# Optimization experiments

Hardware: AMD Instinct MI355X
Metric: run time of the kernel (lower is better)

## Reference

```python
import jax, jax.numpy as jnp
import numpy as np

N_EL = 16
N_NUC = 4
N_FEATS = 32
CUTOFF = 10.0
ION_POT = 0.5
ALPHA = 1.0
BATCH = 32768
HIDDEN = 64
I_IDX, J_IDX = np.triu_indices(N_EL, 1)  # electron pairs i<j
N_PAIRS = N_EL * N_NUC + N_EL * (N_EL - 1) // 2
D_IN = N_PAIRS * N_FEATS


def ssp(x):
    # shifted softplus: softplus(x) - log(2), so ssp(0) = 0
    return jax.nn.softplus(x) - jnp.log(2.0).astype(x.dtype)


def setup_inputs() -> dict:
    key = jax.random.key(0)
    ks = jax.random.split(key, 9)
    rs = jax.random.normal(ks[0], (BATCH, N_EL, 3), jnp.float32) * 2.0
    coords = jax.random.normal(ks[1], (N_NUC, 3), jnp.float32)
    charges = jnp.arange(1, N_NUC + 1, dtype=jnp.float32)
    W1 = jax.random.normal(ks[2], (D_IN, HIDDEN), jnp.float32) / jnp.sqrt(D_IN)
    b1 = jnp.zeros((HIDDEN,), jnp.float32)
    W2 = jax.random.normal(ks[3], (HIDDEN, HIDDEN), jnp.float32) / jnp.sqrt(HIDDEN)
    b2 = jnp.zeros((HIDDEN,), jnp.float32)
    W3 = jax.random.normal(ks[4], (HIDDEN, 1), jnp.float32) / jnp.sqrt(HIDDEN)
    b3 = jnp.zeros((1,), jnp.float32)
    return {"rs": rs, "coords": coords, "charges": charges,
            "W1": W1, "b1": b1, "W2": W2, "b2": b2, "W3": W3, "b3": b3}


def reference(rs, coords, charges, W1, b1, W2, b2, W3, b3):
    B = rs.shape[0]
    # electron-nucleus distances: [B, n_el, n_nuc]
    diff_nuc = rs[:, :, None, :] - coords[None, None, :, :]
    dists_nuc = jnp.sqrt(jnp.sum(diff_nuc * diff_nuc, axis=-1))
    # electron-electron distances for pairs i<j: [B, n_el*(n_el-1)//2]
    diff_el = rs[:, I_IDX, :] - rs[:, J_IDX, :]
    dists_el = jnp.sqrt(jnp.sum(diff_el * diff_el, axis=-1))
    dists = jnp.concatenate([dists_nuc.reshape(B, -1), dists_el], axis=1)  # [B, N_PAIRS]
    # Gaussian distance basis expansion
    qs = jnp.linspace(0.0, 1.0, N_FEATS, dtype=rs.dtype)
    mus = CUTOFF * qs ** 2
    sigmas = (1.0 + CUTOFF * qs) / 7.0
    xs = jnp.exp(-((dists[..., None] - mus) ** 2) / sigmas ** 2)  # [B, N_PAIRS, N_FEATS]
    xs = xs.reshape(B, -1)
    # small MLP with shifted-softplus activations
    h = ssp(xs @ W1 + b1)
    h = ssp(h @ W2 + b2)
    ys = (h @ W3 + b3)[:, 0]
    # nuclear asymptotic factor
    decay = jnp.sqrt(2.0 * ION_POT)
    terms = (charges[None, None, :] * dists_nuc + decay * ALPHA * dists_nuc ** 2) / (1.0 + ALPHA * dists_nuc)
    asymp = jnp.exp(-jnp.sum(terms, axis=(1, 2)))
    return jnp.exp(ys) * asymp
```

## Files before the change

kernel.cpp:

```cpp
#include <hip/hip_runtime.h>
#include <math.h>

#define N_EL    16
#define N_NUC   4
#define N_FEATS 32
#define N_PAIRS 184
#define HIDDEN  64
#define TB      32
#define BLOCK   256
#define DLD     185
#define H1LD    68
#define TPW     23
#define WS_PART_OFF (1 << 19)

typedef int   intx8    __attribute__((ext_vector_type(8)));
typedef float floatx16 __attribute__((ext_vector_type(16)));

__constant__ unsigned char c_I[120] = {
    0,0,0,0,0,0,0,0,0,0,0,0,0,0,0,
    1,1,1,1,1,1,1,1,1,1,1,1,1,1,
    2,2,2,2,2,2,2,2,2,2,2,2,2,
    3,3,3,3,3,3,3,3,3,3,3,3,
    4,4,4,4,4,4,4,4,4,4,4,
    5,5,5,5,5,5,5,5,5,5,
    6,6,6,6,6,6,6,6,6,
    7,7,7,7,7,7,7,7,
    8,8,8,8,8,8,8,
    9,9,9,9,9,9,
    10,10,10,10,10,
    11,11,11,11,
    12,12,12,
    13,13,
    14
};
__constant__ unsigned char c_J[120] = {
    1,2,3,4,5,6,7,8,9,10,11,12,13,14,15,
    2,3,4,5,6,7,8,9,10,11,12,13,14,15,
    3,4,5,6,7,8,9,10,11,12,13,14,15,
    4,5,6,7,8,9,10,11,12,13,14,15,
    5,6,7,8,9,10,11,12,13,14,15,
    6,7,8,9,10,11,12,13,14,15,
    7,8,9,10,11,12,13,14,15,
    8,9,10,11,12,13,14,15,
    9,10,11,12,13,14,15,
    10,11,12,13,14,15,
    11,12,13,14,15,
    12,13,14,15,
    13,14,15,
    14,15,
    15
};

__device__ __forceinline__ float ssp(float x) {
    float a = fabsf(x);
    return fmaxf(x, 0.0f) + log1pf(__expf(-a)) - 0.69314718056f;
}
__device__ __forceinline__ float redg(float v) {
    v += __shfl_xor(v, 1);
    v += __shfl_xor(v, 2);
    v += __shfl_xor(v, 4);
    return v;
}

__global__ __launch_bounds__(256)
void prep_w1_kernel(const float* __restrict__ W1, intx8* __restrict__ ws)
{
    __shared__ float w[2 * N_FEATS * HIDDEN];
    const int t = blockIdx.x;
    const float* src = W1 + (size_t)(2 * t) * (N_FEATS * HIDDEN);
    for (int k = threadIdx.x; k < 2 * N_FEATS * HIDDEN; k += 256) w[k] = src[k];
    __syncthreads();

    const int tid = threadIdx.x;
    if (tid >= 128) return;
    const int lane = tid & 63;
    const int nh   = tid >> 6;
    const int lh   = lane >> 5;
    const int col  = nh * 32 + (lane & 31);
    const int fb   = lh * 16;
    intx8 frag;
#pragma unroll
    for (int r = 0; r < 8; ++r) {
        const int pair = r >> 2;
        const int fo   = fb + ((r & 3) << 2);
        const float v0 = 64.0f * w[(pair * N_FEATS + fo + 0) * 64 + col];
        const float v1 = 64.0f * w[(pair * N_FEATS + fo + 1) * 64 + col];
        const float v2 = 64.0f * w[(pair * N_FEATS + fo + 2) * 64 + col];
        const float v3 = 64.0f * w[(pair * N_FEATS + fo + 3) * 64 + col];
        int d = __builtin_amdgcn_cvt_pk_fp8_f32(v0, v1, 0, false);
        d     = __builtin_amdgcn_cvt_pk_fp8_f32(v2, v3, d, true);
        frag[r] = d;
    }
    ws[(size_t)(t * 2 + nh) * 64 + lane] = frag;
}

__global__ __launch_bounds__(BLOCK)
void wfnet_gemm(const float* __restrict__ rs,
                const float* __restrict__ coords,
                const intx8* __restrict__ ws,
                float* __restrict__ partials)
{
    __shared__ float lds_rs[TB * N_EL * 3];
    __shared__ float lds_dist[TB * DLD];

    const int tid  = threadIdx.x;
    const int wave = tid >> 6;
    const int lane = tid & 63;
    const int m    = lane & 31;
    const int lh   = lane >> 5;

    {
        const float* rs_blk = rs + (size_t)blockIdx.x * (TB * N_EL * 3);
        for (int k = tid; k < TB * N_EL * 3; k += BLOCK) lds_rs[k] = rs_blk[k];
    }
    __syncthreads();

    {
        const int bl = tid >> 3, g = tid & 7;
        const float* myrs = lds_rs + bl * (N_EL * 3);
        float* dst = lds_dist + bl * DLD;
        for (int i = 0; i < 8; ++i) {
            const int p = g + 8 * i;
            const int e = p >> 2, n = p & 3;
            const float dx = myrs[e * 3 + 0] - coords[n * 3 + 0];
            const float dy = myrs[e * 3 + 1] - coords[n * 3 + 1];
            const float dz = myrs[e * 3 + 2] - coords[n * 3 + 2];
            dst[p] = sqrtf(dx * dx + dy * dy + dz * dz);
        }
        for (int i = 0; i < 15; ++i) {
            const int q  = g + 8 * i;
            const int ei = 3 * (int)c_I[q], ej = 3 * (int)c_J[q];
            const float dx = myrs[ei + 0] - myrs[ej + 0];
            const float dy = myrs[ei + 1] - myrs[ej + 1];
            const float dz = myrs[ei + 2] - myrs[ej + 2];
            dst[64 + q] = sqrtf(dx * dx + dy * dy + dz * dz);
        }
    }
    __syncthreads();

    const int f0 = lh * 16;
#define MKC(P, FF) float P##1, P##0; { \
    const float fq = (float)(FF) * (1.0f / 31.0f); \
    const float mu = 10.0f * fq * fq; \
    const float is = 7.0f / (1.0f + 10.0f * fq); \
    P##1 = is * 3.3972871404442143f; \
    P##0 = -mu * P##1; }
    MKC(F0_,  f0 + 0)  MKC(F1_,  f0 + 1)  MKC(F2_,  f0 + 2)  MKC(F3_,  f0 + 3)
    MKC(F4_,  f0 + 4)  MKC(F5_,  f0 + 5)  MKC(F6_,  f0 + 6)  MKC(F7_,  f0 + 7)
    MKC(F8_,  f0 + 8)  MKC(F9_,  f0 + 9)  MKC(F10_, f0 + 10) MKC(F11_, f0 + 11)
    MKC(F12_, f0 + 12) MKC(F13_, f0 + 13) MKC(F14_, f0 + 14) MKC(F15_, f0 + 15)
#undef MKC

    floatx16 accA = {};
    floatx16 accB = {};
    const intx8* wq = ws + ((size_t)(wave * TPW) * 128 + lane);
    const float* drow = lds_dist + m * DLD + wave * (2 * TPW);

#define XZ(dd, P) ({ const float t_ = fmaf(dd, P##1, P##0); fmaf(t_, -t_, 56.5f); })
#define PKD(dd, A, B, C, D) ({ \
    unsigned w_; \
    w_ = __builtin_amdgcn_cvt_pk_u8_f32(XZ(dd, A), 0, 0u); \
    w_ = __builtin_amdgcn_cvt_pk_u8_f32(XZ(dd, B), 1, w_); \
    w_ = __builtin_amdgcn_cvt_pk_u8_f32(XZ(dd, C), 2, w_); \
    w_ = __builtin_amdgcn_cvt_pk_u8_f32(XZ(dd, D), 3, w_); \
    (int)w_; })
#define MKA8(AV, dx0, dx1) \
    intx8 AV; { \
    AV[0] = PKD(dx0, F0_,  F1_,  F2_,  F3_);  \
    AV[1] = PKD(dx0, F4_,  F5_,  F6_,  F7_);  \
    AV[2] = PKD(dx0, F8_,  F9_,  F10_, F11_); \
    AV[3] = PKD(dx0, F12_, F13_, F14_, F15_); \
    AV[4] = PKD(dx1, F0_,  F1_,  F2_,  F3_);  \
    AV[5] = PKD(dx1, F4_,  F5_,  F6_,  F7_);  \
    AV[6] = PKD(dx1, F8_,  F9_,  F10_, F11_); \
    AV[7] = PKD(dx1, F12_, F13_, F14_, F15_); }
#define KROUND(AV, Q0, Q1) { \
    accA = __builtin_amdgcn_mfma_scale_f32_32x32x64_f8f6f4( \
               AV, Q0, accA, 0, 0, 0, 0x7F7F7F7F, 0, 0x79797979); \
    accB = __builtin_amdgcn_mfma_scale_f32_32x32x64_f8f6f4( \
               AV, Q1, accB, 0, 0, 0, 0x7F7F7F7F, 0, 0x79797979); }

    intx8 pA0 = wq[0],   pA1 = wq[64];
    intx8 pB0 = wq[128], pB1 = wq[192];
    float dA0 = drow[0], dA1 = drow[1];
    float dB0 = drow[2], dB1 = drow[3];

#pragma unroll 1
    for (int it = 0; it < 10; ++it) {
        const intx8* wn = wq + 256;
        const float eA0 = drow[4 * it + 4], eA1 = drow[4 * it + 5];
        const float eB0 = drow[4 * it + 6], eB1 = drow[4 * it + 7];

        { MKA8(av, dA0, dA1) KROUND(av, pA0, pA1) }
        pA0 = wn[0]; pA1 = wn[64];

        { MKA8(bv, dB0, dB1) KROUND(bv, pB0, pB1) }
        pB0 = wn[128]; pB1 = wn[192];

        wq = wn;
        dA0 = eA0; dA1 = eA1; dB0 = eB0; dB1 = eB1;
    }
    {
        const intx8* wn = wq + 256;
        const float eA0 = drow[44], eA1 = drow[45];
        { MKA8(av, dA0, dA1) KROUND(av, pA0, pA1) }
        pA0 = wn[0]; pA1 = wn[64];
        { MKA8(bv, dB0, dB1) KROUND(bv, pB0, pB1) }
        { MKA8(cv, eA0, eA1) KROUND(cv, pA0, pA1) }
    }
#undef KROUND
#undef MKA8
#undef PKD
#undef XZ

    float* pdst = partials + ((size_t)blockIdx.x * 4 + wave) * 2048;
#pragma unroll
    for (int rg = 0; rg < 16; ++rg) {
        const int el = (rg & 3) + 8 * (rg >> 2) + 4 * lh;
        pdst[el * 64 + m]      = accA[rg];
        pdst[el * 64 + 32 + m] = accB[rg];
    }
}

__global__ __launch_bounds__(BLOCK)
void wfnet_tail(const float* __restrict__ rs,
                const float* __restrict__ coords,
                const float* __restrict__ charges,
                const float* __restrict__ partials,
                const float* __restrict__ b1,
                const float* __restrict__ W2,
                const float* __restrict__ b2,
                const float* __restrict__ W3,
                const float* __restrict__ b3,
                float* __restrict__ out)
{
    __shared__ float lds_rs[TB * N_EL * 3];
    __shared__ float lds_h1[TB * H1LD];
    __shared__ float lds_w2[HIDDEN * HIDDEN];

    const int tid = threadIdx.x;
    const int el  = tid >> 3;
    const int g   = tid & 7;
    const int b   = blockIdx.x * TB + el;

    {
        const float* rs_blk = rs + (size_t)blockIdx.x * (TB * N_EL * 3);
        for (int k = tid; k < TB * N_EL * 3; k += BLOCK) lds_rs[k] = rs_blk[k];
    }
    {
        float4* dst = (float4*)lds_w2;
        const float4* src = (const float4*)W2;
#pragma unroll
        for (int i = 0; i < 4; ++i) dst[tid + 256 * i] = src[tid + 256 * i];
    }

    {
        const float* pb = partials + (size_t)blockIdx.x * 8192 + el * 64 + g * 8;
        const float4 p00 = ((const float4*)(pb + 0 * 2048))[0];
        const float4 p01 = ((const float4*)(pb + 0 * 2048))[1];
        const float4 p10 = ((const float4*)(pb + 1 * 2048))[0];
        const float4 p11 = ((const float4*)(pb + 1 * 2048))[1];
        const float4 p20 = ((const float4*)(pb + 2 * 2048))[0];
        const float4 p21 = ((const float4*)(pb + 2 * 2048))[1];
        const float4 p30 = ((const float4*)(pb + 3 * 2048))[0];
        const float4 p31 = ((const float4*)(pb + 3 * 2048))[1];
        const float4 ba = ((const float4*)(b1 + g * 8))[0];
        const float4 bb = ((const float4*)(b1 + g * 8))[1];
        float* h1w = lds_h1 + el * H1LD + g * 8;
        h1w[0] = ssp(p00.x + p10.x + p20.x + p30.x + ba.x);
        h1w[1] = ssp(p00.y + p10.y + p20.y + p30.y + ba.y);
        h1w[2] = ssp(p00.z + p10.z + p20.z + p30.z + ba.z);
        h1w[3] = ssp(p00.w + p10.w + p20.w + p30.w + ba.w);
        h1w[4] = ssp(p01.x + p11.x + p21.x + p31.x + bb.x);
        h1w[5] = ssp(p01.y + p11.y + p21.y + p31.y + bb.y);
        h1w[6] = ssp(p01.z + p11.z + p21.z + p31.z + bb.z);
        h1w[7] = ssp(p01.w + p11.w + p21.w + p31.w + bb.w);
    }

    float asy = 0.0f;
    __syncthreads();
    {
        const float* myrs = lds_rs + el * (N_EL * 3);
        const float4 ch = *(const float4*)charges;
#pragma unroll
        for (int i = 0; i < 8; ++i) {
            const int p = g + 8 * i;
            const int e = p >> 2, n = p & 3;
            const float dx = myrs[e * 3 + 0] - coords[n * 3 + 0];
            const float dy = myrs[e * 3 + 1] - coords[n * 3 + 1];
            const float dz = myrs[e * 3 + 2] - coords[n * 3 + 2];
            const float d = sqrtf(dx * dx + dy * dy + dz * dz);
            const float Z = (n < 2) ? ((n == 0) ? ch.x : ch.y)
                                    : ((n == 2) ? ch.z : ch.w);
            asy += (Z * d + d * d) / (1.0f + d);
        }
    }
    asy = redg(asy);

    const float4* __restrict__ W2v = (const float4*)lds_w2;
    const float4* __restrict__ b2v = (const float4*)b2;
    const int wbi = g * 2;
    const float4 b2a = b2v[wbi], b2b = b2v[wbi + 1];
    float s0 = b2a.x, s1 = b2a.y, s2 = b2a.z, s3 = b2a.w;
    float s4 = b2b.x, s5 = b2b.y, s6 = b2b.z, s7 = b2b.w;

    const float* __restrict__ h1row = lds_h1 + el * H1LD;
    for (int k = 0; k < HIDDEN; ++k) {
        const float hk  = h1row[k];
        const float4 wa = W2v[k * 16 + wbi];
        const float4 wb = W2v[k * 16 + wbi + 1];
        s0 = fmaf(hk, wa.x, s0); s1 = fmaf(hk, wa.y, s1);
        s2 = fmaf(hk, wa.z, s2); s3 = fmaf(hk, wa.w, s3);
        s4 = fmaf(hk, wb.x, s4); s5 = fmaf(hk, wb.y, s5);
        s6 = fmaf(hk, wb.z, s6); s7 = fmaf(hk, wb.w, s7);
    }

    const float4* __restrict__ W3v = (const float4*)W3;
    const float4 w3a = W3v[wbi], w3b = W3v[wbi + 1];
    float part = ssp(s0) * w3a.x + ssp(s1) * w3a.y
               + ssp(s2) * w3a.z + ssp(s3) * w3a.w
               + ssp(s4) * w3b.x + ssp(s5) * w3b.y
               + ssp(s6) * w3b.z + ssp(s7) * w3b.w;
    part = redg(part);

    if (g == 0) {
        const float ys = part + b3[0];
        out[b] = __expf(ys) * __expf(-asy);
    }
}

extern "C" void kernel_launch(void* const* d_in, const int* in_sizes, int n_in,
                              void* d_out, int out_size, void* d_ws, size_t ws_size,
                              hipStream_t stream) {
    const float* rs      = (const float*)d_in[0];
    const float* coords  = (const float*)d_in[1];
    const float* charges = (const float*)d_in[2];
    const float* W1      = (const float*)d_in[3];
    const float* b1      = (const float*)d_in[4];
    const float* W2      = (const float*)d_in[5];
    const float* b2      = (const float*)d_in[6];
    const float* W3      = (const float*)d_in[7];
    const float* b3      = (const float*)d_in[8];
    float* out = (float*)d_out;

    const int batch = in_sizes[0] / (N_EL * 3);
    intx8* w1f8     = (intx8*)d_ws;
    float* partials = (float*)((char*)d_ws + WS_PART_OFF);

    prep_w1_kernel<<<N_PAIRS / 2, 256, 0, stream>>>(W1, w1f8);
    wfnet_gemm<<<batch / TB, BLOCK, 0, stream>>>(rs, coords, w1f8, partials);
    wfnet_tail<<<batch / TB, BLOCK, 0, stream>>>(rs, coords, charges, partials,
                                                 b1, W2, b2, W3, b3, out);
}
```

Before: 129.9 us.

## Split GEMM K-loop across eight waves per block and reduce eight partials

Doubles the gemm block to 512 threads so each wave handles about half of its former K-tiles, shortening the per-wave serial MFMA chain and adding more waves per block. The explicit software prefetch of weights and distances is dropped in favour of simple in-loop loads. The distance precompute is redistributed over 16 threads per batch row. The tail kernel now sums eight partial slices instead of four, which doubles the partials traffic written and read through global memory.

```diff
diff --git a/kernel.cpp b/kernel.cpp
--- a/kernel.cpp
+++ b/kernel.cpp
@@ -7,7 +7,7 @@
 #define N_PAIRS 184
 #define HIDDEN  64
 #define TB      32
-#define BLOCK   256
+#define BLOCK   512
 #define DLD     185
 #define H1LD    68
 #define TPW     23
@@ -108,6 +108,8 @@
     const int lane = tid & 63;
     const int m    = lane & 31;
     const int lh   = lane >> 5;
+    const int w4   = wave & 3;
+    const int half = wave >> 2;
 
     {
         const float* rs_blk = rs + (size_t)blockIdx.x * (TB * N_EL * 3);
@@ -116,24 +118,28 @@
     __syncthreads();
 
     {
-        const int bl = tid >> 3, g = tid & 7;
+        const int bl = tid >> 4, g = tid & 15;
         const float* myrs = lds_rs + bl * (N_EL * 3);
         float* dst = lds_dist + bl * DLD;
-        for (int i = 0; i < 8; ++i) {
-            const int p = g + 8 * i;
+#pragma unroll
+        for (int i = 0; i < 4; ++i) {
+            const int p = g + 16 * i;
             const int e = p >> 2, n = p & 3;
             const float dx = myrs[e * 3 + 0] - coords[n * 3 + 0];
             const float dy = myrs[e * 3 + 1] - coords[n * 3 + 1];
             const float dz = myrs[e * 3 + 2] - coords[n * 3 + 2];
             dst[p] = sqrtf(dx * dx + dy * dy + dz * dz);
         }
-        for (int i = 0; i < 15; ++i) {
-            const int q  = g + 8 * i;
-            const int ei = 3 * (int)c_I[q], ej = 3 * (int)c_J[q];
-            const float dx = myrs[ei + 0] - myrs[ej + 0];
-            const float dy = myrs[ei + 1] - myrs[ej + 1];
-            const float dz = myrs[ei + 2] - myrs[ej + 2];
-            dst[64 + q] = sqrtf(dx * dx + dy * dy + dz * dz);
+#pragma unroll
+        for (int i = 0; i < 8; ++i) {
+            const int q = g + 16 * i;
+            if (q < 120) {
+                const int ei = 3 * (int)c_I[q], ej = 3 * (int)c_J[q];
+                const float dx = myrs[ei + 0] - myrs[ej + 0];
+                const float dy = myrs[ei + 1] - myrs[ej + 1];
+                const float dz = myrs[ei + 2] - myrs[ej + 2];
+                dst[64 + q] = sqrtf(dx * dx + dy * dy + dz * dz);
+            }
         }
     }
     __syncthreads();
@@ -153,8 +159,9 @@
 
     floatx16 accA = {};
     floatx16 accB = {};
-    const intx8* wq = ws + ((size_t)(wave * TPW) * 128 + lane);
-    const float* drow = lds_dist + m * DLD + wave * (2 * TPW);
+    const intx8* wq = ws + ((size_t)(23 * w4 + 12 * half) * 128 + lane);
+    const float* drow = lds_dist + m * DLD + 46 * w4 + 24 * half;
+    const int nd = 6 - half;
 
 #define XZ(dd, P) ({ const float t_ = fmaf(dd, P##1, P##0); fmaf(t_, -t_, 56.5f); })
 #define PKD(dd, A, B, C, D) ({ \
@@ -180,40 +187,27 @@
     accB = __builtin_amdgcn_mfma_scale_f32_32x32x64_f8f6f4( \
                AV, Q1, accB, 0, 0, 0, 0x7F7F7F7F, 0, 0x79797979); }
 
-    intx8 pA0 = wq[0],   pA1 = wq[64];
-    intx8 pB0 = wq[128], pB1 = wq[192];
-    float dA0 = drow[0], dA1 = drow[1];
-    float dB0 = drow[2], dB1 = drow[3];
-
 #pragma unroll 1
-    for (int it = 0; it < 10; ++it) {
-        const intx8* wn = wq + 256;
-        const float eA0 = drow[4 * it + 4], eA1 = drow[4 * it + 5];
-        const float eB0 = drow[4 * it + 6], eB1 = drow[4 * it + 7];
-
-        { MKA8(av, dA0, dA1) KROUND(av, pA0, pA1) }
-        pA0 = wn[0]; pA1 = wn[64];
-
-        { MKA8(bv, dB0, dB1) KROUND(bv, pB0, pB1) }
-        pB0 = wn[128]; pB1 = wn[192];
-
-        wq = wn;
-        dA0 = eA0; dA1 = eA1; dB0 = eB0; dB1 = eB1;
-    }
-    {
-        const intx8* wn = wq + 256;
-        const float eA0 = drow[44], eA1 = drow[45];
-        { MKA8(av, dA0, dA1) KROUND(av, pA0, pA1) }
-        pA0 = wn[0]; pA1 = wn[64];
-        { MKA8(bv, dB0, dB1) KROUND(bv, pB0, pB1) }
-        { MKA8(cv, eA0, eA1) KROUND(cv, pA0, pA1) }
+    for (int it = 0; it < nd; ++it) {
+        const intx8 a0 = wq[0],   a1 = wq[64];
+        const intx8 b0 = wq[128], b1 = wq[192];
+        const float d0 = drow[4 * it + 0], d1 = drow[4 * it + 1];
+        const float d2 = drow[4 * it + 2], d3 = drow[4 * it + 3];
+        { MKA8(av, d0, d1) KROUND(av, a0, a1) }
+        { MKA8(bv, d2, d3) KROUND(bv, b0, b1) }
+        wq += 256;
+    }
+    if (half) {
+        const intx8 a0 = wq[0], a1 = wq[64];
+        const float d0 = drow[20], d1 = drow[21];
+        { MKA8(cv, d0, d1) KROUND(cv, a0, a1) }
     }
 #undef KROUND
 #undef MKA8
 #undef PKD
 #undef XZ
 
-    float* pdst = partials + ((size_t)blockIdx.x * 4 + wave) * 2048;
+    float* pdst = partials + ((size_t)blockIdx.x * 8 + wave) * 2048;
 #pragma unroll
     for (int rg = 0; rg < 16; ++rg) {
         const int el = (rg & 3) + 8 * (rg >> 2) + 4 * lh;
@@ -222,7 +216,7 @@
     }
 }
 
-__global__ __launch_bounds__(BLOCK)
+__global__ __launch_bounds__(256)
 void wfnet_tail(const float* __restrict__ rs,
                 const float* __restrict__ coords,
                 const float* __restrict__ charges,
@@ -245,7 +239,7 @@
 
     {
         const float* rs_blk = rs + (size_t)blockIdx.x * (TB * N_EL * 3);
-        for (int k = tid; k < TB * N_EL * 3; k += BLOCK) lds_rs[k] = rs_blk[k];
+        for (int k = tid; k < TB * N_EL * 3; k += 256) lds_rs[k] = rs_blk[k];
     }
     {
         float4* dst = (float4*)lds_w2;
@@ -255,26 +249,26 @@
     }
 
     {
-        const float* pb = partials + (size_t)blockIdx.x * 8192 + el * 64 + g * 8;
-        const float4 p00 = ((const float4*)(pb + 0 * 2048))[0];
-        const float4 p01 = ((const float4*)(pb + 0 * 2048))[1];
-        const float4 p10 = ((const float4*)(pb + 1 * 2048))[0];
-        const float4 p11 = ((const float4*)(pb + 1 * 2048))[1];
-        const float4 p20 = ((const float4*)(pb + 2 * 2048))[0];
-        const float4 p21 = ((const float4*)(pb + 2 * 2048))[1];
-        const float4 p30 = ((const float4*)(pb + 3 * 2048))[0];
-        const float4 p31 = ((const float4*)(pb + 3 * 2048))[1];
+        const float* pb = partials + (size_t)blockIdx.x * 16384 + el * 64 + g * 8;
+        float4 s0 = {0.f, 0.f, 0.f, 0.f}, s1 = {0.f, 0.f, 0.f, 0.f};
+#pragma unroll
+        for (int wv = 0; wv < 8; ++wv) {
+            const float4 a = ((const float4*)(pb + wv * 2048))[0];
+            const float4 c = ((const float4*)(pb + wv * 2048))[1];
+            s0.x += a.x; s0.y += a.y; s0.z += a.z; s0.w += a.w;
+            s1.x += c.x; s1.y += c.y; s1.z += c.z; s1.w += c.w;
+        }
         const float4 ba = ((const float4*)(b1 + g * 8))[0];
         const float4 bb = ((const float4*)(b1 + g * 8))[1];
         float* h1w = lds_h1 + el * H1LD + g * 8;
-        h1w[0] = ssp(p00.x + p10.x + p20.x + p30.x + ba.x);
-        h1w[1] = ssp(p00.y + p10.y + p20.y + p30.y + ba.y);
-        h1w[2] = ssp(p00.z + p10.z + p20.z + p30.z + ba.z);
-        h1w[3] = ssp(p00.w + p10.w + p20.w + p30.w + ba.w);
-        h1w[4] = ssp(p01.x + p11.x + p21.x + p31.x + bb.x);
-        h1w[5] = ssp(p01.y + p11.y + p21.y + p31.y + bb.y);
-        h1w[6] = ssp(p01.z + p11.z + p21.z + p31.z + bb.z);
-        h1w[7] = ssp(p01.w + p11.w + p21.w + p31.w + bb.w);
+        h1w[0] = ssp(s0.x + ba.x);
+        h1w[1] = ssp(s0.y + ba.y);
+        h1w[2] = ssp(s0.z + ba.z);
+        h1w[3] = ssp(s0.w + ba.w);
+        h1w[4] = ssp(s1.x + bb.x);
+        h1w[5] = ssp(s1.y + bb.y);
+        h1w[6] = ssp(s1.z + bb.z);
+        h1w[7] = ssp(s1.w + bb.w);
     }
 
     float asy = 0.0f;
@@ -349,6 +343,6 @@
 
     prep_w1_kernel<<<N_PAIRS / 2, 256, 0, stream>>>(W1, w1f8);
     wfnet_gemm<<<batch / TB, BLOCK, 0, stream>>>(rs, coords, w1f8, partials);
-    wfnet_tail<<<batch / TB, BLOCK, 0, stream>>>(rs, coords, charges, partials,
-                                                 b1, W2, b2, W3, b3, out);
-}
+    wfnet_tail<<<batch / TB, 256, 0, stream>>>(rs, coords, charges, partials,
+                                               b1, W2, b2, W3, b3, out);
+}
```

Result: slower. 137.6 us (+5.9%).
